# Optimization experiments

Measured on AMD Instinct MI355X. Metric: run time of the kernel, lower is better.

## Reference

```python
import jax, jax.numpy as jnp
import numpy as np

EMBED_DIM = 64  # matches init_kwargs embed_dim; used for 1/sqrt(d) scaling


def setup_inputs() -> dict:
    key = jax.random.key(0)
    k1, k2, k3, k4 = jax.random.split(key, 4)
    N1, N2, C, B = 8192, 8192, EMBED_DIM, 8
    query = jax.random.normal(k1, (N1, C), dtype=jnp.float32)
    key_value = jax.random.normal(k2, (N2, C), dtype=jnp.float32)
    # sorted batch indices so per-batch concat order == input row order
    query_coors = jnp.sort(jax.random.randint(k3, (N1,), 0, B))
    key_value_coors = jnp.sort(jax.random.randint(k4, (N2,), 0, B))
    return {
        "query": query,
        "key_value": key_value,
        "query_coors": query_coors,
        "key_value_coors": key_value_coors,
    }


def reference(query, key_value, query_coors, key_value_coors):
    # Per-batch attention: each query row attends only to key_value rows with
    # the same batch index. Equivalent to the original per-batch loop +
    # chunked softmax(QK^T/sqrt(d)) V, expressed as one masked attention.
    # Dropout is identity (eval mode) for a deterministic correctness baseline.
    scale = 1.0 / jnp.sqrt(jnp.asarray(EMBED_DIM, dtype=query.dtype))
    scores = jnp.einsum("nc,mc->nm", query, key_value) * scale  # [N1, N2]
    same_batch = query_coors[:, None] == key_value_coors[None, :]
    neg_inf = jnp.asarray(-jnp.inf, dtype=scores.dtype)
    scores = jnp.where(same_batch, scores, neg_inf)
    attn = jax.nn.softmax(scores, axis=-1)  # softmax within each batch segment
    out = jnp.einsum("nm,mc->nc", attn, key_value)  # [N1, C]
    return out
```

## Files before the change

kernel.cpp:

```cpp
#include <hip/hip_runtime.h>
#include <hip/hip_bf16.h>

typedef __attribute__((ext_vector_type(8))) short bf16x8;
typedef __attribute__((ext_vector_type(4))) unsigned short u16x4;
typedef __attribute__((ext_vector_type(4))) float f32x4;

#define NEG_INF (-__builtin_inff())
#define QSCALE (0.125f * 1.4426950408889634f)
#define CONST_M 12.0f

static __device__ __forceinline__ unsigned short f2bf(float x) {
  union { float f; unsigned u; } v; v.f = x;
  unsigned r = (v.u + 0x7fffu + ((v.u >> 16) & 1u)) >> 16;
  return (unsigned short)r;
}

__global__ __launch_bounds__(256) void prep_kv_kernel(
    const float* __restrict__ kv, const int* __restrict__ kvc,
    unsigned short* __restrict__ kvb, unsigned short* __restrict__ kvt,
    int* __restrict__ seg, int nkv) {
  __shared__ unsigned short tile[16][64];
  const int nb8 = gridDim.x >> 3;
  const int bp = ((gridDim.x & 7) == 0) ? ((blockIdx.x & 7) * nb8 + (blockIdx.x >> 3))
                                        : blockIdx.x;
  const int rowbase = bp * 16;
  const int t = threadIdx.x;
  if (t < 16) {
    int i = rowbase + t;
    if (i < nkv) {
      int c = kvc[i];
      int cp = (i == 0) ? -1 : kvc[i - 1];
      if (c != cp) {
        for (int b = cp + 1; b <= c; ++b) seg[b] = i;
        if (i == 0) for (int b = 0; b < c; ++b) seg[8 + b] = 0;
      }
      int cn = (i == nkv - 1) ? 8 : kvc[i + 1];
      if (c != cn) {
        for (int b = c; b < cn; ++b) seg[8 + b] = i + 1;
        if (i == nkv - 1) for (int b = c + 1; b < 8; ++b) seg[b] = nkv;
      }
    }
  }
  const int r = t >> 4;
  const int c = (t & 15) * 4;
  float4 a = *(const float4*)(kv + (size_t)(rowbase + r) * 64 + c);
  u16x4 v4;
  v4[0] = f2bf(a.x); v4[1] = f2bf(a.y); v4[2] = f2bf(a.z); v4[3] = f2bf(a.w);
  *(u16x4*)(kvb + (size_t)(rowbase + r) * 64 + c) = v4;
  *(u16x4*)&tile[r][c] = v4;
  __syncthreads();
  const int d = t & 63;
  const int k0 = (t >> 6) * 4;
  u16x4 wv;
#pragma unroll
  for (int j = 0; j < 4; ++j) wv[j] = tile[k0 + j][d];
  const int blk = rowbase >> 5;
  const int kbase = (rowbase & 31) + k0;
  *(u16x4*)(kvt + (size_t)blk * 2048 + d * 32 + kbase) = wv;
}

#define LOADK(P, kvx)                                                          \
  {                                                                            \
    const unsigned short* kb_ = kvb + (((size_t)((kvx) + rowoff)) << 6) + g8;  \
    k##P##0 = *(const bf16x8*)(kb_);                                           \
    k##P##1 = *(const bf16x8*)(kb_ + 32);                                      \
    k##P##2 = *(const bf16x8*)(kb_ + 256);                                     \
    k##P##3 = *(const bf16x8*)(kb_ + 256 + 32);                                \
  }

#define SOFTMAX_PACK(s0_, s1_, mS, lS, loS, hiS, pa_)                          \
  {                                                                            \
    float v_[8];                                                               \
    if (full_) {                                                               \
      _Pragma("unroll") for (int r = 0; r < 4; ++r) {                          \
        v_[r] = s0_[r]; v_[4 + r] = s1_[r];                                    \
      }                                                                        \
    } else {                                                                   \
      _Pragma("unroll") for (int r = 0; r < 4; ++r) {                          \
        v_[r]     = (k0_ + r     >= loS && k0_ + r     < hiS) ? s0_[r] : NEG_INF; \
        v_[4 + r] = (k0_ + r + 4 >= loS && k0_ + r + 4 < hiS) ? s1_[r] : NEG_INF; \
      }                                                                        \
    }                                                                          \
    float t_ = fmaxf(fmaxf(fmaxf(v_[0], v_[1]), fmaxf(v_[2], v_[3])),          \
                     fmaxf(fmaxf(v_[4], v_[5]), fmaxf(v_[6], v_[7])));         \
    if (__builtin_expect(__any(t_ > mS), 0)) {                                 \
      float tt_ = fmaxf(t_, __shfl_xor(t_, 16));                               \
      tt_ = fmaxf(tt_, __shfl_xor(tt_, 32));                                   \
      float mn_ = fmaxf(mS, tt_);                                              \
      float f_ = __builtin_exp2f(mS - mn_);                                    \
      lS *= f_;                                                                \
      _Pragma("unroll") for (int r = 0; r < 4; ++r) {                          \
        acc##pa_##0[r] *= f_; acc##pa_##1[r] *= f_;                            \
        acc##pa_##2[r] *= f_; acc##pa_##3[r] *= f_;                            \
      }                                                                        \
      mS = mn_;                                                                \
    }                                                                          \
    float e_[8];                                                               \
    _Pragma("unroll") for (int i = 0; i < 8; ++i)                              \
      e_[i] = __builtin_exp2f(v_[i] - mS);                                     \
    lS += (((e_[0] + e_[1]) + (e_[2] + e_[3])) +                               \
           ((e_[4] + e_[5]) + (e_[6] + e_[7])));                               \
    _Pragma("unroll") for (int j = 0; j < 8; ++j)                              \
      pab##pa_[j] = (short)f2bf(e_[j]);                                        \
  }

#define STEP(P, kvx)                                                           \
  {                                                                            \
    const int kv0_ = (kvx);                                                    \
    const unsigned short* vb_ = kvt + (((size_t)kv0_ >> 5) << 11) + q16 * 32 + g8; \
    bf16x8 vf0_ = *(const bf16x8*)(vb_);                                       \
    bf16x8 vf1_ = *(const bf16x8*)(vb_ + 512);                                 \
    bf16x8 vf2_ = *(const bf16x8*)(vb_ + 1024);                                \
    bf16x8 vf3_ = *(const bf16x8*)(vb_ + 1536);                                \
    f32x4 z_ = {0, 0, 0, 0};                                                   \
    __builtin_amdgcn_s_setprio(1);                                             \
    f32x4 s00 = __builtin_amdgcn_mfma_f32_16x16x32_bf16(k##P##0, q00, z_, 0, 0, 0); \
    s00 = __builtin_amdgcn_mfma_f32_16x16x32_bf16(k##P##1, q01, s00, 0, 0, 0); \
    f32x4 s01 = __builtin_amdgcn_mfma_f32_16x16x32_bf16(k##P##2, q00, z_, 0, 0, 0); \
    s01 = __builtin_amdgcn_mfma_f32_16x16x32_bf16(k##P##3, q01, s01, 0, 0, 0); \
    f32x4 s10 = __builtin_amdgcn_mfma_f32_16x16x32_bf16(k##P##0, q10, z_, 0, 0, 0); \
    s10 = __builtin_amdgcn_mfma_f32_16x16x32_bf16(k##P##1, q11, s10, 0, 0, 0); \
    f32x4 s11 = __builtin_amdgcn_mfma_f32_16x16x32_bf16(k##P##2, q10, z_, 0, 0, 0); \
    s11 = __builtin_amdgcn_mfma_f32_16x16x32_bf16(k##P##3, q11, s11, 0, 0, 0); \
    __builtin_amdgcn_s_setprio(0);                                             \
    const bool full_ = uniformb && (kv0_ >= kv_lo) && (kv0_ + 32 <= kv_hi);    \
    const int k0_ = kv0_ + g8;                                                 \
    bf16x8 pab0, pab1;                                                         \
    SOFTMAX_PACK(s00, s01, m0, l0, lo0, hi0, 0)                                \
    SOFTMAX_PACK(s10, s11, m1, l1, lo1, hi1, 1)                                \
    __builtin_amdgcn_s_setprio(1);                                             \
    acc00 = __builtin_amdgcn_mfma_f32_16x16x32_bf16(vf0_, pab0, acc00, 0, 0, 0); \
    acc01 = __builtin_amdgcn_mfma_f32_16x16x32_bf16(vf1_, pab0, acc01, 0, 0, 0); \
    acc02 = __builtin_amdgcn_mfma_f32_16x16x32_bf16(vf2_, pab0, acc02, 0, 0, 0); \
    acc03 = __builtin_amdgcn_mfma_f32_16x16x32_bf16(vf3_, pab0, acc03, 0, 0, 0); \
    acc10 = __builtin_amdgcn_mfma_f32_16x16x32_bf16(vf0_, pab1, acc10, 0, 0, 0); \
    acc11 = __builtin_amdgcn_mfma_f32_16x16x32_bf16(vf1_, pab1, acc11, 0, 0, 0); \
    acc12 = __builtin_amdgcn_mfma_f32_16x16x32_bf16(vf2_, pab1, acc12, 0, 0, 0); \
    acc13 = __builtin_amdgcn_mfma_f32_16x16x32_bf16(vf3_, pab1, acc13, 0, 0, 0); \
    __builtin_amdgcn_s_setprio(0);                                             \
  }

__global__ __launch_bounds__(256, 2) void attn_kernel(
    const float* __restrict__ qf,
    const unsigned short* __restrict__ kvb,
    const unsigned short* __restrict__ kvt,
    const int* __restrict__ qc,
    const int* __restrict__ seg,
    float* __restrict__ pacc,
    float2* __restrict__ pml,
    int n2, int ncl2)
{
  const int nc = 1 << ncl2;
  const int per8 = gridDim.x >> 3;
  const int ii = ((gridDim.x & 7) == 0) ? ((blockIdx.x & 7) * per8 + (blockIdx.x >> 3))
                                        : blockIdx.x;
  const int qt = ii >> ncl2;
  const int c  = ii & (nc - 1);
  const int qbase = qt << 7;

  const int w = threadIdx.x >> 6;
  const int lane = threadIdx.x & 63;
  const int q16 = lane & 15;
  const int g = lane >> 4;
  const int g8 = g * 8;
  const int q0w = qbase + w * 32;

  const int myb0 = qc[q0w + q16];
  const int myb1 = qc[q0w + 16 + q16];
  const int lo0 = seg[myb0], hi0 = seg[8 + myb0];
  const int lo1 = seg[myb1], hi1 = seg[8 + myb1];
  const int bfirst = __shfl(myb0, 0);
  const int blast  = __shfl(myb1, 15);
  const int kv_lo  = __shfl(lo0, 0);
  const int kv_hi  = __shfl(hi1, 15);
  const bool uniformb = (bfirst == blast);

  bf16x8 q00, q01, q10, q11;
  {
    const float* qr0 = qf + (size_t)(q0w + q16) * 64 + g8;
    const float* qr1 = qf + (size_t)(q0w + 16 + q16) * 64 + g8;
    float4 a0 = *(const float4*)(qr0),     a1 = *(const float4*)(qr0 + 4);
    float4 a2 = *(const float4*)(qr0 + 32), a3 = *(const float4*)(qr0 + 36);
    float4 b0 = *(const float4*)(qr1),     b1 = *(const float4*)(qr1 + 4);
    float4 b2 = *(const float4*)(qr1 + 32), b3 = *(const float4*)(qr1 + 36);
    q00[0]=(short)f2bf(a0.x*QSCALE); q00[1]=(short)f2bf(a0.y*QSCALE);
    q00[2]=(short)f2bf(a0.z*QSCALE); q00[3]=(short)f2bf(a0.w*QSCALE);
    q00[4]=(short)f2bf(a1.x*QSCALE); q00[5]=(short)f2bf(a1.y*QSCALE);
    q00[6]=(short)f2bf(a1.z*QSCALE); q00[7]=(short)f2bf(a1.w*QSCALE);
    q01[0]=(short)f2bf(a2.x*QSCALE); q01[1]=(short)f2bf(a2.y*QSCALE);
    q01[2]=(short)f2bf(a2.z*QSCALE); q01[3]=(short)f2bf(a2.w*QSCALE);
    q01[4]=(short)f2bf(a3.x*QSCALE); q01[5]=(short)f2bf(a3.y*QSCALE);
    q01[6]=(short)f2bf(a3.z*QSCALE); q01[7]=(short)f2bf(a3.w*QSCALE);
    q10[0]=(short)f2bf(b0.x*QSCALE); q10[1]=(short)f2bf(b0.y*QSCALE);
    q10[2]=(short)f2bf(b0.z*QSCALE); q10[3]=(short)f2bf(b0.w*QSCALE);
    q10[4]=(short)f2bf(b1.x*QSCALE); q10[5]=(short)f2bf(b1.y*QSCALE);
    q10[6]=(short)f2bf(b1.z*QSCALE); q10[7]=(short)f2bf(b1.w*QSCALE);
    q11[0]=(short)f2bf(b2.x*QSCALE); q11[1]=(short)f2bf(b2.y*QSCALE);
    q11[2]=(short)f2bf(b2.z*QSCALE); q11[3]=(short)f2bf(b2.w*QSCALE);
    q11[4]=(short)f2bf(b3.x*QSCALE); q11[5]=(short)f2bf(b3.y*QSCALE);
    q11[6]=(short)f2bf(b3.z*QSCALE); q11[7]=(short)f2bf(b3.w*QSCALE);
  }

  const int base = kv_lo & ~31;
  const int nblk = (kv_hi - base + 31) >> 5;
  const int b0i = (nblk * c) >> ncl2;
  const int b1i = (nblk * (c + 1)) >> ncl2;

  const int rowoff = ((q16 >> 2) << 3) + (q16 & 3);

  f32x4 acc00 = {0,0,0,0}, acc01 = {0,0,0,0}, acc02 = {0,0,0,0}, acc03 = {0,0,0,0};
  f32x4 acc10 = {0,0,0,0}, acc11 = {0,0,0,0}, acc12 = {0,0,0,0}, acc13 = {0,0,0,0};
  float m0 = CONST_M, l0 = 0.0f;
  float m1 = CONST_M, l1 = 0.0f;

  bf16x8 kA0, kA1, kA2, kA3, kB0, kB1, kB2, kB3;
  int b = b0i;
  if (b < b1i) {
    LOADK(A, base + b * 32);
    while (true) {
      if (b + 1 < b1i) LOADK(B, base + (b + 1) * 32);
      STEP(A, base + b * 32);
      ++b; if (b >= b1i) break;
      if (b + 1 < b1i) LOADK(A, base + (b + 1) * 32);
      STEP(B, base + b * 32);
      ++b; if (b >= b1i) break;
    }
  }

  l0 += __shfl_xor(l0, 16); l0 += __shfl_xor(l0, 32);
  l1 += __shfl_xor(l1, 16); l1 += __shfl_xor(l1, 32);

  const int row0 = q0w + q16;
  const int row1 = q0w + 16 + q16;
  float* pr0 = pacc + ((size_t)row0 * nc + c) * 64;
  float* pr1 = pacc + ((size_t)row1 * nc + c) * 64;
  *(f32x4*)(pr0 + 0  + g * 4) = acc00;
  *(f32x4*)(pr0 + 16 + g * 4) = acc01;
  *(f32x4*)(pr0 + 32 + g * 4) = acc02;
  *(f32x4*)(pr0 + 48 + g * 4) = acc03;
  *(f32x4*)(pr1 + 0  + g * 4) = acc10;
  *(f32x4*)(pr1 + 16 + g * 4) = acc11;
  *(f32x4*)(pr1 + 32 + g * 4) = acc12;
  *(f32x4*)(pr1 + 48 + g * 4) = acc13;
  if (g == 0) {
    float2 v0; v0.x = m0; v0.y = l0;
    float2 v1; v1.x = m1; v1.y = l1;
    pml[(size_t)row0 * nc + c] = v0;
    pml[(size_t)row1 * nc + c] = v1;
  }
}

__global__ __launch_bounds__(256) void merge_kernel(
    const float* __restrict__ pacc, const float2* __restrict__ pml,
    float* __restrict__ out, int ncl2)
{
  const int nc = 1 << ncl2;
  const int nb8 = gridDim.x >> 3;
  const int bq = ((gridDim.x & 7) == 0) ? ((blockIdx.x & 7) * nb8 + (blockIdx.x >> 3))
                                        : blockIdx.x;
  const int q0 = bq * 16;
  const int t = threadIdx.x;
  const int i = t >> 4;
  const int c0 = (t & 15) * 4;
  const int R = q0 + i;

  float mm[8], ll[8], sc[8];
  float mstar = NEG_INF;
#pragma unroll
  for (int cc = 0; cc < 8; ++cc) if (cc < nc) {
    float2 v = pml[(size_t)R * nc + cc];
    mm[cc] = v.x; ll[cc] = v.y;
    mstar = fmaxf(mstar, v.x);
  }
  float L = 0.0f;
#pragma unroll
  for (int cc = 0; cc < 8; ++cc) if (cc < nc) {
    sc[cc] = __builtin_exp2f(mm[cc] - mstar);
    L += sc[cc] * ll[cc];
  }
  float inv = (L > 0.0f) ? 1.0f / L : 0.0f;
  f32x4 num = {0, 0, 0, 0};
#pragma unroll
  for (int cc = 0; cc < 8; ++cc) if (cc < nc) {
    f32x4 a = *(const f32x4*)&pacc[((size_t)R * nc + cc) * 64 + c0];
    num[0] += sc[cc] * a[0]; num[1] += sc[cc] * a[1];
    num[2] += sc[cc] * a[2]; num[3] += sc[cc] * a[3];
  }
  f32x4 o;
  o[0] = num[0] * inv; o[1] = num[1] * inv;
  o[2] = num[2] * inv; o[3] = num[3] * inv;
  *(f32x4*)&out[(size_t)R * 64 + c0] = o;
}

extern "C" void kernel_launch(void* const* d_in, const int* in_sizes, int n_in,
                              void* d_out, int out_size, void* d_ws, size_t ws_size,
                              hipStream_t stream) {
  const float* q  = (const float*)d_in[0];
  const float* kv = (const float*)d_in[1];
  const int* qc   = (const int*)d_in[2];
  const int* kvc  = (const int*)d_in[3];
  float* out = (float*)d_out;

  const int C = 64;
  const int n1 = in_sizes[0] / C;
  const int n2 = in_sizes[1] / C;

  const size_t fixed = (size_t)n2 * C * 2 * 2 + 4096;
  int ncl2 = 0;
  if (ws_size >= fixed + (size_t)n1 * 8 * (64 * 4 + 8)) ncl2 = 3;
  else if (ws_size >= fixed + (size_t)n1 * 4 * (64 * 4 + 8)) ncl2 = 2;
  else if (ws_size >= fixed + (size_t)n1 * 2 * (64 * 4 + 8)) ncl2 = 1;
  const int nc = 1 << ncl2;

  char* ws = (char*)d_ws;
  size_t off = 0;
  unsigned short* kvb = (unsigned short*)(ws + off); off += (size_t)n2 * C * 2;
  unsigned short* kvt = (unsigned short*)(ws + off); off += (size_t)n2 * C * 2;
  int* seg = (int*)(ws + off); off += 4096;
  float* pacc = (float*)(ws + off); off += (size_t)n1 * nc * 64 * 4;
  float2* pml = (float2*)(ws + off);

  prep_kv_kernel<<<n2 / 16, 256, 0, stream>>>(kv, kvc, kvb, kvt, seg, n2);
  attn_kernel<<<(n1 / 128) * nc, 256, 0, stream>>>(q, kvb, kvt, qc, seg, pacc, pml, n2, ncl2);
  merge_kernel<<<n1 / 16, 256, 0, stream>>>(pacc, pml, out, ncl2);
}
```

Baseline: 29.65 us.

## Process 64 query rows per wave to reuse K/V fragments across four tiles

Each wave now handles four 16-row query tiles instead of two, so every loaded K and V fragment feeds twice as many MFMAs. The block tile doubles to 256 queries, halving the attention grid, and occupancy hints drop to one block per SIMD to allow the larger register footprint. Softmax and the PV MFMAs are interleaved per tile to shorten live ranges. The minimum split count is forced to at least 2, which risks overrunning the workspace if it is small. Fewer blocks and higher register pressure may reduce latency hiding.

```diff
diff --git a/kernel.cpp b/kernel.cpp
--- a/kernel.cpp
+++ b/kernel.cpp
@@ -68,8 +68,30 @@
     k##P##3 = *(const bf16x8*)(kb_ + 256 + 32);                                \
   }
 
-#define SOFTMAX_PACK(s0_, s1_, mS, lS, loS, hiS, pa_)                          \
-  {                                                                            \
+#define LOADQ(S, qrow_)                                                        \
+  {                                                                            \
+    const float* qr_ = (qrow_);                                                \
+    float4 a0 = *(const float4*)(qr_),      a1 = *(const float4*)(qr_ + 4);    \
+    float4 a2 = *(const float4*)(qr_ + 32), a3 = *(const float4*)(qr_ + 36);   \
+    q##S##0[0]=(short)f2bf(a0.x*QSCALE); q##S##0[1]=(short)f2bf(a0.y*QSCALE);  \
+    q##S##0[2]=(short)f2bf(a0.z*QSCALE); q##S##0[3]=(short)f2bf(a0.w*QSCALE);  \
+    q##S##0[4]=(short)f2bf(a1.x*QSCALE); q##S##0[5]=(short)f2bf(a1.y*QSCALE);  \
+    q##S##0[6]=(short)f2bf(a1.z*QSCALE); q##S##0[7]=(short)f2bf(a1.w*QSCALE);  \
+    q##S##1[0]=(short)f2bf(a2.x*QSCALE); q##S##1[1]=(short)f2bf(a2.y*QSCALE);  \
+    q##S##1[2]=(short)f2bf(a2.z*QSCALE); q##S##1[3]=(short)f2bf(a2.w*QSCALE);  \
+    q##S##1[4]=(short)f2bf(a3.x*QSCALE); q##S##1[5]=(short)f2bf(a3.y*QSCALE);  \
+    q##S##1[6]=(short)f2bf(a3.z*QSCALE); q##S##1[7]=(short)f2bf(a3.w*QSCALE);  \
+  }
+
+#define PROCESS(P, S)                                                          \
+  {                                                                            \
+    f32x4 z_ = {0, 0, 0, 0};                                                   \
+    __builtin_amdgcn_s_setprio(1);                                             \
+    f32x4 s0_ = __builtin_amdgcn_mfma_f32_16x16x32_bf16(k##P##0, q##S##0, z_, 0, 0, 0); \
+    s0_ = __builtin_amdgcn_mfma_f32_16x16x32_bf16(k##P##1, q##S##1, s0_, 0, 0, 0); \
+    f32x4 s1_ = __builtin_amdgcn_mfma_f32_16x16x32_bf16(k##P##2, q##S##0, z_, 0, 0, 0); \
+    s1_ = __builtin_amdgcn_mfma_f32_16x16x32_bf16(k##P##3, q##S##1, s1_, 0, 0, 0); \
+    __builtin_amdgcn_s_setprio(0);                                             \
     float v_[8];                                                               \
     if (full_) {                                                               \
       _Pragma("unroll") for (int r = 0; r < 4; ++r) {                          \
@@ -77,31 +99,37 @@
       }                                                                        \
     } else {                                                                   \
       _Pragma("unroll") for (int r = 0; r < 4; ++r) {                          \
-        v_[r]     = (k0_ + r     >= loS && k0_ + r     < hiS) ? s0_[r] : NEG_INF; \
-        v_[4 + r] = (k0_ + r + 4 >= loS && k0_ + r + 4 < hiS) ? s1_[r] : NEG_INF; \
+        v_[r]     = (k0_ + r     >= lo##S && k0_ + r     < hi##S) ? s0_[r] : NEG_INF; \
+        v_[4 + r] = (k0_ + r + 4 >= lo##S && k0_ + r + 4 < hi##S) ? s1_[r] : NEG_INF; \
       }                                                                        \
     }                                                                          \
     float t_ = fmaxf(fmaxf(fmaxf(v_[0], v_[1]), fmaxf(v_[2], v_[3])),          \
                      fmaxf(fmaxf(v_[4], v_[5]), fmaxf(v_[6], v_[7])));         \
-    if (__builtin_expect(__any(t_ > mS), 0)) {                                 \
+    if (__builtin_expect(__any(t_ > m##S), 0)) {                               \
       float tt_ = fmaxf(t_, __shfl_xor(t_, 16));                               \
       tt_ = fmaxf(tt_, __shfl_xor(tt_, 32));                                   \
-      float mn_ = fmaxf(mS, tt_);                                              \
-      float f_ = __builtin_exp2f(mS - mn_);                                    \
-      lS *= f_;                                                                \
+      float mn_ = fmaxf(m##S, tt_);                                            \
+      float f_ = __builtin_exp2f(m##S - mn_);                                  \
+      l##S *= f_;                                                              \
       _Pragma("unroll") for (int r = 0; r < 4; ++r) {                          \
-        acc##pa_##0[r] *= f_; acc##pa_##1[r] *= f_;                            \
-        acc##pa_##2[r] *= f_; acc##pa_##3[r] *= f_;                            \
+        acc##S##0[r] *= f_; acc##S##1[r] *= f_;                                \
+        acc##S##2[r] *= f_; acc##S##3[r] *= f_;                                \
       }                                                                        \
-      mS = mn_;                                                                \
+      m##S = mn_;                                                              \
     }                                                                          \
     float e_[8];                                                               \
     _Pragma("unroll") for (int i = 0; i < 8; ++i)                              \
-      e_[i] = __builtin_exp2f(v_[i] - mS);                                     \
-    lS += (((e_[0] + e_[1]) + (e_[2] + e_[3])) +                               \
-           ((e_[4] + e_[5]) + (e_[6] + e_[7])));                               \
-    _Pragma("unroll") for (int j = 0; j < 8; ++j)                              \
-      pab##pa_[j] = (short)f2bf(e_[j]);                                        \
+      e_[i] = __builtin_exp2f(v_[i] - m##S);                                   \
+    l##S += (((e_[0] + e_[1]) + (e_[2] + e_[3])) +                             \
+             ((e_[4] + e_[5]) + (e_[6] + e_[7])));                             \
+    bf16x8 pa_;                                                                \
+    _Pragma("unroll") for (int j = 0; j < 8; ++j) pa_[j] = (short)f2bf(e_[j]); \
+    __builtin_amdgcn_s_setprio(1);                                             \
+    acc##S##0 = __builtin_amdgcn_mfma_f32_16x16x32_bf16(vf0_, pa_, acc##S##0, 0, 0, 0); \
+    acc##S##1 = __builtin_amdgcn_mfma_f32_16x16x32_bf16(vf1_, pa_, acc##S##1, 0, 0, 0); \
+    acc##S##2 = __builtin_amdgcn_mfma_f32_16x16x32_bf16(vf2_, pa_, acc##S##2, 0, 0, 0); \
+    acc##S##3 = __builtin_amdgcn_mfma_f32_16x16x32_bf16(vf3_, pa_, acc##S##3, 0, 0, 0); \
+    __builtin_amdgcn_s_setprio(0);                                             \
   }
 
 #define STEP(P, kvx)                                                           \
@@ -112,35 +140,15 @@
     bf16x8 vf1_ = *(const bf16x8*)(vb_ + 512);                                 \
     bf16x8 vf2_ = *(const bf16x8*)(vb_ + 1024);                                \
     bf16x8 vf3_ = *(const bf16x8*)(vb_ + 1536);                                \
-    f32x4 z_ = {0, 0, 0, 0};                                                   \
-    __builtin_amdgcn_s_setprio(1);                                             \
-    f32x4 s00 = __builtin_amdgcn_mfma_f32_16x16x32_bf16(k##P##0, q00, z_, 0, 0, 0); \
-    s00 = __builtin_amdgcn_mfma_f32_16x16x32_bf16(k##P##1, q01, s00, 0, 0, 0); \
-    f32x4 s01 = __builtin_amdgcn_mfma_f32_16x16x32_bf16(k##P##2, q00, z_, 0, 0, 0); \
-    s01 = __builtin_amdgcn_mfma_f32_16x16x32_bf16(k##P##3, q01, s01, 0, 0, 0); \
-    f32x4 s10 = __builtin_amdgcn_mfma_f32_16x16x32_bf16(k##P##0, q10, z_, 0, 0, 0); \
-    s10 = __builtin_amdgcn_mfma_f32_16x16x32_bf16(k##P##1, q11, s10, 0, 0, 0); \
-    f32x4 s11 = __builtin_amdgcn_mfma_f32_16x16x32_bf16(k##P##2, q10, z_, 0, 0, 0); \
-    s11 = __builtin_amdgcn_mfma_f32_16x16x32_bf16(k##P##3, q11, s11, 0, 0, 0); \
-    __builtin_amdgcn_s_setprio(0);                                             \
     const bool full_ = uniformb && (kv0_ >= kv_lo) && (kv0_ + 32 <= kv_hi);    \
     const int k0_ = kv0_ + g8;                                                 \
-    bf16x8 pab0, pab1;                                                         \
-    SOFTMAX_PACK(s00, s01, m0, l0, lo0, hi0, 0)                                \
-    SOFTMAX_PACK(s10, s11, m1, l1, lo1, hi1, 1)                                \
-    __builtin_amdgcn_s_setprio(1);                                             \
-    acc00 = __builtin_amdgcn_mfma_f32_16x16x32_bf16(vf0_, pab0, acc00, 0, 0, 0); \
-    acc01 = __builtin_amdgcn_mfma_f32_16x16x32_bf16(vf1_, pab0, acc01, 0, 0, 0); \
-    acc02 = __builtin_amdgcn_mfma_f32_16x16x32_bf16(vf2_, pab0, acc02, 0, 0, 0); \
-    acc03 = __builtin_amdgcn_mfma_f32_16x16x32_bf16(vf3_, pab0, acc03, 0, 0, 0); \
-    acc10 = __builtin_amdgcn_mfma_f32_16x16x32_bf16(vf0_, pab1, acc10, 0, 0, 0); \
-    acc11 = __builtin_amdgcn_mfma_f32_16x16x32_bf16(vf1_, pab1, acc11, 0, 0, 0); \
-    acc12 = __builtin_amdgcn_mfma_f32_16x16x32_bf16(vf2_, pab1, acc12, 0, 0, 0); \
-    acc13 = __builtin_amdgcn_mfma_f32_16x16x32_bf16(vf3_, pab1, acc13, 0, 0, 0); \
-    __builtin_amdgcn_s_setprio(0);                                             \
-  }
-
-__global__ __launch_bounds__(256, 2) void attn_kernel(
+    PROCESS(P, 0)                                                              \
+    PROCESS(P, 1)                                                              \
+    PROCESS(P, 2)                                                              \
+    PROCESS(P, 3)                                                              \
+  }
+
+__global__ __launch_bounds__(256, 1) void attn_kernel(
     const float* __restrict__ qf,
     const unsigned short* __restrict__ kvb,
     const unsigned short* __restrict__ kvt,
@@ -156,50 +164,34 @@
                                         : blockIdx.x;
   const int qt = ii >> ncl2;
   const int c  = ii & (nc - 1);
-  const int qbase = qt << 7;
+  const int qbase = qt << 8;
 
   const int w = threadIdx.x >> 6;
   const int lane = threadIdx.x & 63;
   const int q16 = lane & 15;
   const int g = lane >> 4;
   const int g8 = g * 8;
-  const int q0w = qbase + w * 32;
+  const int q0w = qbase + w * 64;
 
   const int myb0 = qc[q0w + q16];
   const int myb1 = qc[q0w + 16 + q16];
+  const int myb2 = qc[q0w + 32 + q16];
+  const int myb3 = qc[q0w + 48 + q16];
   const int lo0 = seg[myb0], hi0 = seg[8 + myb0];
   const int lo1 = seg[myb1], hi1 = seg[8 + myb1];
+  const int lo2 = seg[myb2], hi2 = seg[8 + myb2];
+  const int lo3 = seg[myb3], hi3 = seg[8 + myb3];
   const int bfirst = __shfl(myb0, 0);
-  const int blast  = __shfl(myb1, 15);
+  const int blast  = __shfl(myb3, 15);
   const int kv_lo  = __shfl(lo0, 0);
-  const int kv_hi  = __shfl(hi1, 15);
+  const int kv_hi  = __shfl(hi3, 15);
   const bool uniformb = (bfirst == blast);
 
-  bf16x8 q00, q01, q10, q11;
-  {
-    const float* qr0 = qf + (size_t)(q0w + q16) * 64 + g8;
-    const float* qr1 = qf + (size_t)(q0w + 16 + q16) * 64 + g8;
-    float4 a0 = *(const float4*)(qr0),     a1 = *(const float4*)(qr0 + 4);
-    float4 a2 = *(const float4*)(qr0 + 32), a3 = *(const float4*)(qr0 + 36);
-    float4 b0 = *(const float4*)(qr1),     b1 = *(const float4*)(qr1 + 4);
-    float4 b2 = *(const float4*)(qr1 + 32), b3 = *(const float4*)(qr1 + 36);
-    q00[0]=(short)f2bf(a0.x*QSCALE); q00[1]=(short)f2bf(a0.y*QSCALE);
-    q00[2]=(short)f2bf(a0.z*QSCALE); q00[3]=(short)f2bf(a0.w*QSCALE);
-    q00[4]=(short)f2bf(a1.x*QSCALE); q00[5]=(short)f2bf(a1.y*QSCALE);
-    q00[6]=(short)f2bf(a1.z*QSCALE); q00[7]=(short)f2bf(a1.w*QSCALE);
-    q01[0]=(short)f2bf(a2.x*QSCALE); q01[1]=(short)f2bf(a2.y*QSCALE);
-    q01[2]=(short)f2bf(a2.z*QSCALE); q01[3]=(short)f2bf(a2.w*QSCALE);
-    q01[4]=(short)f2bf(a3.x*QSCALE); q01[5]=(short)f2bf(a3.y*QSCALE);
-    q01[6]=(short)f2bf(a3.z*QSCALE); q01[7]=(short)f2bf(a3.w*QSCALE);
-    q10[0]=(short)f2bf(b0.x*QSCALE); q10[1]=(short)f2bf(b0.y*QSCALE);
-    q10[2]=(short)f2bf(b0.z*QSCALE); q10[3]=(short)f2bf(b0.w*QSCALE);
-    q10[4]=(short)f2bf(b1.x*QSCALE); q10[5]=(short)f2bf(b1.y*QSCALE);
-    q10[6]=(short)f2bf(b1.z*QSCALE); q10[7]=(short)f2bf(b1.w*QSCALE);
-    q11[0]=(short)f2bf(b2.x*QSCALE); q11[1]=(short)f2bf(b2.y*QSCALE);
-    q11[2]=(short)f2bf(b2.z*QSCALE); q11[3]=(short)f2bf(b2.w*QSCALE);
-    q11[4]=(short)f2bf(b3.x*QSCALE); q11[5]=(short)f2bf(b3.y*QSCALE);
-    q11[6]=(short)f2bf(b3.z*QSCALE); q11[7]=(short)f2bf(b3.w*QSCALE);
-  }
+  bf16x8 q00, q01, q10, q11, q20, q21, q30, q31;
+  LOADQ(0, qf + (size_t)(q0w + q16) * 64 + g8);
+  LOADQ(1, qf + (size_t)(q0w + 16 + q16) * 64 + g8);
+  LOADQ(2, qf + (size_t)(q0w + 32 + q16) * 64 + g8);
+  LOADQ(3, qf + (size_t)(q0w + 48 + q16) * 64 + g8);
 
   const int base = kv_lo & ~31;
   const int nblk = (kv_hi - base + 31) >> 5;
@@ -210,8 +202,12 @@
 
   f32x4 acc00 = {0,0,0,0}, acc01 = {0,0,0,0}, acc02 = {0,0,0,0}, acc03 = {0,0,0,0};
   f32x4 acc10 = {0,0,0,0}, acc11 = {0,0,0,0}, acc12 = {0,0,0,0}, acc13 = {0,0,0,0};
+  f32x4 acc20 = {0,0,0,0}, acc21 = {0,0,0,0}, acc22 = {0,0,0,0}, acc23 = {0,0,0,0};
+  f32x4 acc30 = {0,0,0,0}, acc31 = {0,0,0,0}, acc32 = {0,0,0,0}, acc33 = {0,0,0,0};
   float m0 = CONST_M, l0 = 0.0f;
   float m1 = CONST_M, l1 = 0.0f;
+  float m2 = CONST_M, l2 = 0.0f;
+  float m3 = CONST_M, l3 = 0.0f;
 
   bf16x8 kA0, kA1, kA2, kA3, kB0, kB1, kB2, kB3;
   int b = b0i;
@@ -229,25 +225,27 @@
 
   l0 += __shfl_xor(l0, 16); l0 += __shfl_xor(l0, 32);
   l1 += __shfl_xor(l1, 16); l1 += __shfl_xor(l1, 32);
-
-  const int row0 = q0w + q16;
-  const int row1 = q0w + 16 + q16;
-  float* pr0 = pacc + ((size_t)row0 * nc + c) * 64;
-  float* pr1 = pacc + ((size_t)row1 * nc + c) * 64;
-  *(f32x4*)(pr0 + 0  + g * 4) = acc00;
-  *(f32x4*)(pr0 + 16 + g * 4) = acc01;
-  *(f32x4*)(pr0 + 32 + g * 4) = acc02;
-  *(f32x4*)(pr0 + 48 + g * 4) = acc03;
-  *(f32x4*)(pr1 + 0  + g * 4) = acc10;
-  *(f32x4*)(pr1 + 16 + g * 4) = acc11;
-  *(f32x4*)(pr1 + 32 + g * 4) = acc12;
-  *(f32x4*)(pr1 + 48 + g * 4) = acc13;
-  if (g == 0) {
-    float2 v0; v0.x = m0; v0.y = l0;
-    float2 v1; v1.x = m1; v1.y = l1;
-    pml[(size_t)row0 * nc + c] = v0;
-    pml[(size_t)row1 * nc + c] = v1;
-  }
+  l2 += __shfl_xor(l2, 16); l2 += __shfl_xor(l2, 32);
+  l3 += __shfl_xor(l3, 16); l3 += __shfl_xor(l3, 32);
+
+#define WRITEOUT(S, off_)                                                      \
+  {                                                                            \
+    const int row_ = q0w + (off_) + q16;                                       \
+    float* pr_ = pacc + ((size_t)row_ * nc + c) * 64;                          \
+    *(f32x4*)(pr_ + 0  + g * 4) = acc##S##0;                                   \
+    *(f32x4*)(pr_ + 16 + g * 4) = acc##S##1;                                   \
+    *(f32x4*)(pr_ + 32 + g * 4) = acc##S##2;                                   \
+    *(f32x4*)(pr_ + 48 + g * 4) = acc##S##3;                                   \
+    if (g == 0) {                                                              \
+      float2 v_; v_.x = m##S; v_.y = l##S;                                     \
+      pml[(size_t)row_ * nc + c] = v_;                                         \
+    }                                                                          \
+  }
+  WRITEOUT(0, 0)
+  WRITEOUT(1, 16)
+  WRITEOUT(2, 32)
+  WRITEOUT(3, 48)
+#undef WRITEOUT
 }
 
 __global__ __launch_bounds__(256) void merge_kernel(
@@ -306,10 +304,9 @@
   const int n2 = in_sizes[1] / C;
 
   const size_t fixed = (size_t)n2 * C * 2 * 2 + 4096;
-  int ncl2 = 0;
+  int ncl2 = 1;
   if (ws_size >= fixed + (size_t)n1 * 8 * (64 * 4 + 8)) ncl2 = 3;
   else if (ws_size >= fixed + (size_t)n1 * 4 * (64 * 4 + 8)) ncl2 = 2;
-  else if (ws_size >= fixed + (size_t)n1 * 2 * (64 * 4 + 8)) ncl2 = 1;
   const int nc = 1 << ncl2;
 
   char* ws = (char*)d_ws;
@@ -321,6 +318,6 @@
   float2* pml = (float2*)(ws + off);
 
   prep_kv_kernel<<<n2 / 16, 256, 0, stream>>>(kv, kvc, kvb, kvt, seg, n2);
-  attn_kernel<<<(n1 / 128) * nc, 256, 0, stream>>>(q, kvb, kvt, qc, seg, pacc, pml, n2, ncl2);
+  attn_kernel<<<(n1 / 256) * nc, 256, 0, stream>>>(q, kvb, kvt, qc, seg, pacc, pml, n2, ncl2);
   merge_kernel<<<n1 / 16, 256, 0, stream>>>(pacc, pml, out, ncl2);
 }
```

After: 39.20 us. 32.2% more time.
